# Kernel tuning notes

Measured on AMD Instinct MI355X. Metric: run time of the kernel, lower is better.

## Reference

```python
import jax, jax.numpy as jnp
import numpy as np
from functools import partial

B, T, I, H, S = 256, 512, 128, 256, 4  # batch, seq_len, input_size, hidden_size, num_segments


def setup_inputs() -> dict:
    key = jax.random.key(0)
    ks = jax.random.split(key, 6)
    x = jax.random.normal(ks[0], (B, T, I), dtype=jnp.float32)
    # variable-length sequences so segment indexing floor(t*S/len) is exercised
    lengths = jax.random.randint(ks[1], (B,), T // 2, T + 1)
    mask = jnp.arange(T)[None, :] < lengths[:, None]  # [B, T] bool
    s = 1.0 / np.sqrt(H)  # torch LSTMCell init: U(-1/sqrt(H), 1/sqrt(H))
    W_ih = jax.random.uniform(ks[2], (S, 4 * H, I), minval=-s, maxval=s, dtype=jnp.float32)
    W_hh = jax.random.uniform(ks[3], (S, 4 * H, H), minval=-s, maxval=s, dtype=jnp.float32)
    b_ih = jax.random.uniform(ks[4], (S, 4 * H), minval=-s, maxval=s, dtype=jnp.float32)
    b_hh = jax.random.uniform(ks[5], (S, 4 * H), minval=-s, maxval=s, dtype=jnp.float32)
    return {"x": x, "mask": mask, "W_ih": W_ih, "W_hh": W_hh, "b_ih": b_ih, "b_hh": b_hh}


def _shift_lstm(x, mask, W_ih, W_hh, b_ih, b_hh):
    # dropout is identity in eval mode
    Bb, Tt, _ = x.shape
    lengths = jnp.maximum(mask.astype(jnp.int32).sum(-1), 1)  # clamp_min(1)
    t = jnp.arange(Tt)
    seg = jnp.minimum((t[None, :] * S) // lengths[:, None], S - 1)  # [B, T]
    bias = (b_ih + b_hh)[None]  # [1, S, 4H]

    def step(carry, inputs):
        h, c = carry
        x_t, seg_t, valid = inputs  # [B,I], [B], [B]
        # gates for every segment cell, then pick each sample's segment
        gates = (jnp.einsum('bi,soi->bso', x_t, W_ih)
                 + jnp.einsum('bh,soh->bso', h, W_hh) + bias)  # [B, S, 4H]
        g = jnp.take_along_axis(gates, seg_t[:, None, None], axis=1)[:, 0, :]  # [B, 4H]
        i_g, f_g, g_g, o_g = jnp.split(g, 4, axis=-1)  # torch LSTMCell gate order i,f,g,o
        c_new = jax.nn.sigmoid(f_g) * c + jax.nn.sigmoid(i_g) * jnp.tanh(g_g)
        h_new = jax.nn.sigmoid(o_g) * jnp.tanh(c_new)
        v = valid[:, None]
        h = jnp.where(v, h_new, h)
        c = jnp.where(v, c_new, c)
        out = jnp.where(v, h, jnp.zeros_like(h))  # padded steps stay zero
        return (h, c), out

    h0 = jnp.zeros((Bb, H), dtype=x.dtype)
    c0 = jnp.zeros((Bb, H), dtype=x.dtype)
    xs = (x.transpose(1, 0, 2), seg.T, mask.T)
    _, outs = jax.lax.scan(step, (h0, c0), xs)
    outputs = outs.transpose(1, 0, 2)  # [B, T, H]
    last_idx = (lengths - 1)[:, None, None]
    last_outputs = jnp.take_along_axis(outputs, last_idx, axis=1)[:, 0, :]  # [B, H]
    return outputs, last_outputs


def reference(x, mask, W_ih, W_hh, b_ih, b_hh):
    return _shift_lstm(x, mask, W_ih, W_hh, b_ih, b_hh)
```

## Files before the change

kernel.cpp:

```cpp
#include <hip/hip_runtime.h>
#include <math.h>

#define Bb 256
#define Tt 512
#define Ii 128
#define Hh 256
#define Ss 4
#define G4 1024

#define TILE 8

typedef _Float16 half2t __attribute__((ext_vector_type(2)));
union W16 { uint4 u; half2t h[4]; };
union CV8 { _Float16 h[4]; uint2 u; };

__device__ __forceinline__ float dot8(uint4 w, uint4 hv, float acc) {
  W16 a; a.u = w; W16 b; b.u = hv;
#if __has_builtin(__builtin_amdgcn_fdot2)
  acc = __builtin_amdgcn_fdot2(a.h[0], b.h[0], acc, false);
  acc = __builtin_amdgcn_fdot2(a.h[1], b.h[1], acc, false);
  acc = __builtin_amdgcn_fdot2(a.h[2], b.h[2], acc, false);
  acc = __builtin_amdgcn_fdot2(a.h[3], b.h[3], acc, false);
#else
#pragma unroll
  for (int k = 0; k < 4; k++)
    acc += (float)a.h[k].x * (float)b.h[k].x + (float)a.h[k].y * (float)b.h[k].y;
#endif
  return acc;
}

__global__ void k_len(const int* __restrict__ mask, int* __restrict__ len) {
  int b = blockIdx.x, tid = threadIdx.x;
  int c = (mask[b * Tt + tid] != 0) + (mask[b * Tt + 256 + tid] != 0);
#pragma unroll
  for (int off = 32; off > 0; off >>= 1) c += __shfl_down(c, off, 64);
  __shared__ int red[4];
  if ((tid & 63) == 0) red[tid >> 6] = c;
  __syncthreads();
  if (tid == 0) {
    int t = red[0] + red[1] + red[2] + red[3];
    len[b] = t < 1 ? 1 : t;
  }
}

__global__ void k_tr(const float* __restrict__ W_ih, const float* __restrict__ W_hh,
                     uint4* __restrict__ wt_hh16, uint4* __restrict__ wt_ih16) {
  int id = blockIdx.x * blockDim.x + threadIdx.x;
  const int NH16 = Ss * 32 * G4;
  const int NI16 = Ss * 16 * G4;
  if (id < NH16) {
    int o = id % G4, i8 = (id / G4) % 32, s = id / (G4 * 32);
    const float* src = W_hh + ((size_t)(s * G4 + o)) * Hh + 8 * i8;
    W16 w;
#pragma unroll
    for (int k = 0; k < 4; k++) {
      w.h[k].x = (_Float16)src[2 * k];
      w.h[k].y = (_Float16)src[2 * k + 1];
    }
    wt_hh16[id] = w.u;
  } else if (id < NH16 + NI16) {
    int id3 = id - NH16;
    int o = id3 % G4, i8 = (id3 / G4) % 16, s = id3 / (G4 * 16);
    const float* src = W_ih + ((size_t)(s * G4 + o)) * Ii + 8 * i8;
    W16 w;
#pragma unroll
    for (int k = 0; k < 4; k++) {
      w.h[k].x = (_Float16)src[2 * k];
      w.h[k].y = (_Float16)src[2 * k + 1];
    }
    wt_ih16[id3] = w.u;
  }
}

__global__ __launch_bounds__(512) void k_fused(
    const float* __restrict__ x, const uint4* __restrict__ wt_hh16,
    const uint4* __restrict__ wt_ih16, const float* __restrict__ b_ih,
    const float* __restrict__ b_hh, const int* __restrict__ len,
    float* __restrict__ out) {
  __shared__ __align__(16) uint4 lds_w[19 * 512];
  __shared__ __align__(16) _Float16 xs[TILE * Ii];
  __shared__ __align__(16) _Float16 h_h[Hh];
  __shared__ float f_sh[Hh];
  __shared__ float o_sh[Hh];
  const int b = blockIdx.x;
  const int tid = threadIdx.x;
  const int u = tid & 255;
  const int pr = tid >> 8;
  const int r0 = u + pr * 256;
  const int r1 = r0 + 512;
  const int L = len[b];
  const int tb1 = (L + 3) >> 2;
  const int tb2 = (2 * L + 3) >> 2;
  const int tb3 = (3 * L + 3) >> 2;
  if (pr == 0) h_h[u] = (_Float16)0.f;
  float c = 0.f;
  float* outb = out + (size_t)b * Tt * Hh;
  float* lastb = out + (size_t)Bb * Tt * Hh + (size_t)b * Hh;
  const uint4* h4 = (const uint4*)h_h;
  const uint4* xs4 = (const uint4*)xs;
  uint4 w0v[6];
  uint4 w1v[4];
  int s_cur = -1;
  float xg0[TILE], xg1[TILE];

  for (int t0 = 0; t0 < L; t0 += TILE) {
    if (tid < TILE * Ii / 4) {
      float4 xf = ((const float4*)(x + ((size_t)b * Tt + t0) * Ii))[tid];
      CV8 cv;
      cv.h[0] = (_Float16)xf.x;
      cv.h[1] = (_Float16)xf.y;
      cv.h[2] = (_Float16)xf.z;
      cv.h[3] = (_Float16)xf.w;
      ((uint2*)xs)[tid] = cv.u;
    }
    __syncthreads();

    int segv[TILE];
#pragma unroll
    for (int tt = 0; tt < TILE; tt++) {
      int t = t0 + tt;
      segv[tt] = (t >= tb1) + (t >= tb2) + (t >= tb3);
    }
    const int s_lo = segv[0];
    const int tlast = (t0 + TILE - 1 < L) ? (t0 + TILE - 1) : (L - 1);
    const int s_hi = (tlast >= tb1) + (tlast >= tb2) + (tlast >= tb3);

    for (int s = s_lo; s <= s_hi; s++) {
      float acc0[TILE], acc1[TILE];
#pragma unroll
      for (int tt = 0; tt < TILE; tt++) { acc0[tt] = 0.f; acc1[tt] = 0.f; }
      const uint4* wbi = wt_ih16 + ((size_t)s * 16) * G4;
#pragma unroll 2
      for (int i8 = 0; i8 < 16; i8++) {
        uint4 w0 = wbi[(size_t)i8 * G4 + r0];
        uint4 w1 = wbi[(size_t)i8 * G4 + r1];
#pragma unroll
        for (int tt = 0; tt < TILE; tt++) {
          uint4 hv = xs4[tt * 16 + i8];
          acc0[tt] = dot8(w0, hv, acc0[tt]);
          acc1[tt] = dot8(w1, hv, acc1[tt]);
        }
      }
      float bias0 = b_ih[s * G4 + r0] + b_hh[s * G4 + r0];
      float bias1 = b_ih[s * G4 + r1] + b_hh[s * G4 + r1];
#pragma unroll
      for (int tt = 0; tt < TILE; tt++) {
        if (segv[tt] == s) {
          xg0[tt] = acc0[tt] + bias0;
          xg1[tt] = acc1[tt] + bias1;
        }
      }
    }

#pragma unroll
    for (int tt = 0; tt < TILE; tt++) {
      const int t = t0 + tt;
      if (t < L) {
        const int s = segv[tt];
        if (s != s_cur) {
          s_cur = s;
          const uint4* wb0 = wt_hh16 + (size_t)s * 32 * G4 + r0;
          const uint4* wb1 = wt_hh16 + (size_t)s * 32 * G4 + r1;
#pragma unroll
          for (int j = 0; j < 10; j++) lds_w[j * 512 + tid] = wb0[(size_t)j * G4];
#pragma unroll
          for (int j = 0; j < 9; j++)
            lds_w[(10 + j) * 512 + tid] = wb1[(size_t)j * G4];
#pragma unroll
          for (int k = 0; k < 6; k++) w0v[k] = wb0[(size_t)(10 + k) * G4];
#pragma unroll
          for (int k = 0; k < 4; k++) w1v[k] = wb1[(size_t)(9 + k) * G4];
        }
        const uint4* wbs0 = wt_hh16 + (size_t)s_cur * 32 * G4 + r0;
        const uint4* wbs1 = wt_hh16 + (size_t)s_cur * 32 * G4 + r1;
        uint4 sA[16], sB[19];
        sB[0] = wbs1[(size_t)13 * G4];
        sB[1] = wbs1[(size_t)14 * G4];
        sB[2] = wbs1[(size_t)15 * G4];
        sB[3] = wbs1[(size_t)16 * G4];
        sA[0] = wbs0[(size_t)16 * G4];
        sA[1] = wbs0[(size_t)17 * G4];
        float a0 = xg0[tt], a1 = xg1[tt];
        float a0b = 0.f, a1b = 0.f;
        __syncthreads();
#pragma unroll
        for (int i8 = 0; i8 < 32; i8++) {
          if (i8 == 2) sB[4] = wbs1[(size_t)17 * G4];
          if (i8 == 5) sB[5] = wbs1[(size_t)18 * G4];
          if (i8 == 8) sB[6] = wbs1[(size_t)19 * G4];
          if (i8 == 11) sB[7] = wbs1[(size_t)20 * G4];
          if (i8 >= 13 && i8 <= 23) {
            sB[i8 - 5] = wbs1[(size_t)(i8 + 8) * G4];
            if (i8 >= 14) sA[i8 - 12] = wbs0[(size_t)(i8 + 4) * G4];
          }
          if (i8 == 24) sA[12] = wbs0[(size_t)28 * G4];
          if (i8 == 25) sA[13] = wbs0[(size_t)29 * G4];
          if (i8 == 26) sA[14] = wbs0[(size_t)30 * G4];
          if (i8 == 27) sA[15] = wbs0[(size_t)31 * G4];
          uint4 hv = h4[i8];
          uint4 wA = (i8 < 10) ? lds_w[i8 * 512 + tid]
                   : (i8 < 16) ? w0v[i8 - 10] : sA[i8 - 16];
          uint4 wB = (i8 < 9) ? lds_w[(10 + i8) * 512 + tid]
                   : (i8 < 13) ? w1v[i8 - 9] : sB[i8 - 13];
          if (i8 & 1) { a0b = dot8(wA, hv, a0b); a1b = dot8(wB, hv, a1b); }
          else        { a0  = dot8(wA, hv, a0 ); a1  = dot8(wB, hv, a1 ); }
        }
        a0 += a0b;
        a1 += a1b;
        if (pr == 1) {
          f_sh[u] = 1.f / (1.f + expf(-a0));
          o_sh[u] = 1.f / (1.f + expf(-a1));
        }
        __syncthreads();
        if (pr == 0) {
          float ig = 1.f / (1.f + expf(-a0));
          float gg = tanhf(a1);
          c = f_sh[u] * c + ig * gg;
          float h = o_sh[u] * tanhf(c);
          h_h[u] = (_Float16)h;
          outb[(size_t)t * Hh + u] = h;
          if (t == L - 1) lastb[u] = h;
        }
      }
    }
  }
  {
    const int ztotal = (Tt - L) * (Hh / 4);
    float4* zb = (float4*)(outb + (size_t)L * Hh);
    float4 z; z.x = z.y = z.z = z.w = 0.f;
    for (int i = tid; i < ztotal; i += 512) zb[i] = z;
  }
}

extern "C" void kernel_launch(void* const* d_in, const int* in_sizes, int n_in,
                              void* d_out, int out_size, void* d_ws, size_t ws_size,
                              hipStream_t stream) {
  const float* x = (const float*)d_in[0];
  const int* mask = (const int*)d_in[1];
  const float* W_ih = (const float*)d_in[2];
  const float* W_hh = (const float*)d_in[3];
  const float* b_ih = (const float*)d_in[4];
  const float* b_hh = (const float*)d_in[5];
  float* out = (float*)d_out;
  char* ws = (char*)d_ws;

  const size_t HH16_OFF = 0;
  const size_t HH16_BYTES = (size_t)Ss * 32 * G4 * 16;
  const size_t IH16_OFF = HH16_OFF + HH16_BYTES;
  const size_t IH16_BYTES = (size_t)Ss * 16 * G4 * 16;
  const size_t LEN_OFF = IH16_OFF + IH16_BYTES;

  uint4* wt_hh16 = (uint4*)(ws + HH16_OFF);
  uint4* wt_ih16 = (uint4*)(ws + IH16_OFF);
  int* len = (int*)(ws + LEN_OFF);

  k_len<<<Bb, 256, 0, stream>>>(mask, len);
  k_tr<<<768, 256, 0, stream>>>(W_ih, W_hh, wt_hh16, wt_ih16);
  k_fused<<<Bb, 512, 0, stream>>>(x, wt_hh16, wt_ih16, b_ih, b_hh, len, out);
}
```

Measured before the change: 2.143 ms.

## Pair length-sorted sequences per block to share recurrent weight loads

Adds a rank-sort kernel that orders batch items by length, then has each block process two adjacent-length sequences at once. When both sequences are in the same segment, each W_hh weight fetch feeds two dot products, which halves weight traffic per step and halves the grid to 128 blocks. When the segments differ, a slow path reads both segment weight sets straight from global memory. Risks include longer per-step latency, lower occupancy from the smaller grid, and extra register pressure.

```diff
diff --git a/kernel.cpp b/kernel.cpp
--- a/kernel.cpp
+++ b/kernel.cpp
@@ -7,8 +7,8 @@
 #define Hh 256
 #define Ss 4
 #define G4 1024
-
 #define TILE 8
+
 
 typedef _Float16 half2t __attribute__((ext_vector_type(2)));
 union W16 { uint4 u; half2t h[4]; };
@@ -29,6 +29,8 @@
   return acc;
 }
 
+__device__ __forceinline__ float sigf(float x) { return 1.f / (1.f + expf(-x)); }
+
 __global__ void k_len(const int* __restrict__ mask, int* __restrict__ len) {
   int b = blockIdx.x, tid = threadIdx.x;
   int c = (mask[b * Tt + tid] != 0) + (mask[b * Tt + 256 + tid] != 0);
@@ -41,6 +43,19 @@
     int t = red[0] + red[1] + red[2] + red[3];
     len[b] = t < 1 ? 1 : t;
   }
+}
+
+__global__ void k_sort(const int* __restrict__ len, int* __restrict__ perm) {
+  __shared__ int l[Bb];
+  int tid = threadIdx.x;
+  l[tid] = len[tid];
+  __syncthreads();
+  int me = l[tid], r = 0;
+  for (int j = 0; j < Bb; j++) {
+    int lj = l[j];
+    r += (lj < me) || (lj == me && j < tid);
+  }
+  perm[r] = tid;
 }
 
 __global__ void k_tr(const float* __restrict__ W_ih, const float* __restrict__ W_hh,
@@ -76,78 +91,106 @@
     const float* __restrict__ x, const uint4* __restrict__ wt_hh16,
     const uint4* __restrict__ wt_ih16, const float* __restrict__ b_ih,
     const float* __restrict__ b_hh, const int* __restrict__ len,
-    float* __restrict__ out) {
-  __shared__ __align__(16) uint4 lds_w[19 * 512];
-  __shared__ __align__(16) _Float16 xs[TILE * Ii];
-  __shared__ __align__(16) _Float16 h_h[Hh];
-  __shared__ float f_sh[Hh];
-  __shared__ float o_sh[Hh];
-  const int b = blockIdx.x;
+    const int* __restrict__ perm, float* __restrict__ out) {
+  __shared__ __align__(16) uint4 lds_w[18 * 512];
+  __shared__ __align__(16) _Float16 xs[2][TILE * Ii];
+  __shared__ __align__(16) _Float16 h1_h[Hh], h2_h[Hh];
+  __shared__ float fo_sh[2][2][Hh];
+  const int g = blockIdx.x;
   const int tid = threadIdx.x;
   const int u = tid & 255;
   const int pr = tid >> 8;
   const int r0 = u + pr * 256;
   const int r1 = r0 + 512;
-  const int L = len[b];
-  const int tb1 = (L + 3) >> 2;
-  const int tb2 = (2 * L + 3) >> 2;
-  const int tb3 = (3 * L + 3) >> 2;
-  if (pr == 0) h_h[u] = (_Float16)0.f;
-  float c = 0.f;
-  float* outb = out + (size_t)b * Tt * Hh;
-  float* lastb = out + (size_t)Bb * Tt * Hh + (size_t)b * Hh;
-  const uint4* h4 = (const uint4*)h_h;
-  const uint4* xs4 = (const uint4*)xs;
-  uint4 w0v[6];
-  uint4 w1v[4];
+  const int b1 = perm[2 * g], b2 = perm[2 * g + 1];
+  const int L1 = len[b1], L2v = len[b2];
+  const int A1 = (L1 + 3) >> 2, A2 = (2 * L1 + 3) >> 2, A3 = (3 * L1 + 3) >> 2;
+  const int C1 = (L2v + 3) >> 2, C2 = (2 * L2v + 3) >> 2, C3 = (3 * L2v + 3) >> 2;
+  if (tid < 256) { h1_h[tid] = (_Float16)0.f; }
+  else { h2_h[tid - 256] = (_Float16)0.f; }
+  float c1 = 0.f, c2 = 0.f;
+  float* out1 = out + (size_t)b1 * Tt * Hh;
+  float* out2 = out + (size_t)b2 * Tt * Hh;
+  float* last1 = out + (size_t)Bb * Tt * Hh + (size_t)b1 * Hh;
+  float* last2 = out + (size_t)Bb * Tt * Hh + (size_t)b2 * Hh;
+  const uint4* h4a = (const uint4*)h1_h;
+  const uint4* h4b = (const uint4*)h2_h;
+  const uint4* xs4a = (const uint4*)xs[0];
+  const uint4* xs4b = (const uint4*)xs[1];
   int s_cur = -1;
-  float xg0[TILE], xg1[TILE];
-
-  for (int t0 = 0; t0 < L; t0 += TILE) {
-    if (tid < TILE * Ii / 4) {
-      float4 xf = ((const float4*)(x + ((size_t)b * Tt + t0) * Ii))[tid];
+  float xg0_1[TILE], xg1_1[TILE], xg0_2[TILE], xg1_2[TILE];
+
+  for (int t0 = 0; t0 < L2v; t0 += TILE) {
+    {
+      int m = tid >> 8, f = tid & 255;
+      const float* xb = x + ((size_t)(m ? b2 : b1) * Tt + t0) * Ii;
+      float4 xf = ((const float4*)xb)[f];
       CV8 cv;
       cv.h[0] = (_Float16)xf.x;
       cv.h[1] = (_Float16)xf.y;
       cv.h[2] = (_Float16)xf.z;
       cv.h[3] = (_Float16)xf.w;
-      ((uint2*)xs)[tid] = cv.u;
+      ((uint2*)xs[m])[f] = cv.u;
     }
     __syncthreads();
 
-    int segv[TILE];
-#pragma unroll
-    for (int tt = 0; tt < TILE; tt++) {
-      int t = t0 + tt;
-      segv[tt] = (t >= tb1) + (t >= tb2) + (t >= tb3);
-    }
-    const int s_lo = segv[0];
-    const int tlast = (t0 + TILE - 1 < L) ? (t0 + TILE - 1) : (L - 1);
-    const int s_hi = (tlast >= tb1) + (tlast >= tb2) + (tlast >= tb3);
-
-    for (int s = s_lo; s <= s_hi; s++) {
-      float acc0[TILE], acc1[TILE];
-#pragma unroll
-      for (int tt = 0; tt < TILE; tt++) { acc0[tt] = 0.f; acc1[tt] = 0.f; }
-      const uint4* wbi = wt_ih16 + ((size_t)s * 16) * G4;
+    if (t0 < L1) {
+      int s_lo = (t0 >= A1) + (t0 >= A2) + (t0 >= A3);
+      int te = t0 + TILE - 1;
+      int s_hi = (te >= A1) + (te >= A2) + (te >= A3);
+      for (int s = s_lo; s <= s_hi; s++) {
+        float acc0[TILE], acc1[TILE];
+#pragma unroll
+        for (int tt = 0; tt < TILE; tt++) { acc0[tt] = 0.f; acc1[tt] = 0.f; }
+        const uint4* wbi = wt_ih16 + ((size_t)s * 16) * G4;
 #pragma unroll 2
-      for (int i8 = 0; i8 < 16; i8++) {
-        uint4 w0 = wbi[(size_t)i8 * G4 + r0];
-        uint4 w1 = wbi[(size_t)i8 * G4 + r1];
+        for (int i8 = 0; i8 < 16; i8++) {
+          uint4 w0 = wbi[(size_t)i8 * G4 + r0];
+          uint4 w1 = wbi[(size_t)i8 * G4 + r1];
+#pragma unroll
+          for (int tt = 0; tt < TILE; tt++) {
+            uint4 hv = xs4a[tt * 16 + i8];
+            acc0[tt] = dot8(w0, hv, acc0[tt]);
+            acc1[tt] = dot8(w1, hv, acc1[tt]);
+          }
+        }
+        float bias0 = b_ih[s * G4 + r0] + b_hh[s * G4 + r0];
+        float bias1 = b_ih[s * G4 + r1] + b_hh[s * G4 + r1];
 #pragma unroll
         for (int tt = 0; tt < TILE; tt++) {
-          uint4 hv = xs4[tt * 16 + i8];
-          acc0[tt] = dot8(w0, hv, acc0[tt]);
-          acc1[tt] = dot8(w1, hv, acc1[tt]);
+          int t = t0 + tt;
+          int sg = (t >= A1) + (t >= A2) + (t >= A3);
+          if (sg == s) { xg0_1[tt] = acc0[tt] + bias0; xg1_1[tt] = acc1[tt] + bias1; }
         }
       }
-      float bias0 = b_ih[s * G4 + r0] + b_hh[s * G4 + r0];
-      float bias1 = b_ih[s * G4 + r1] + b_hh[s * G4 + r1];
-#pragma unroll
-      for (int tt = 0; tt < TILE; tt++) {
-        if (segv[tt] == s) {
-          xg0[tt] = acc0[tt] + bias0;
-          xg1[tt] = acc1[tt] + bias1;
+    }
+    {
+      int s_lo = (t0 >= C1) + (t0 >= C2) + (t0 >= C3);
+      int te = t0 + TILE - 1;
+      int s_hi = (te >= C1) + (te >= C2) + (te >= C3);
+      for (int s = s_lo; s <= s_hi; s++) {
+        float acc0[TILE], acc1[TILE];
+#pragma unroll
+        for (int tt = 0; tt < TILE; tt++) { acc0[tt] = 0.f; acc1[tt] = 0.f; }
+        const uint4* wbi = wt_ih16 + ((size_t)s * 16) * G4;
+#pragma unroll 2
+        for (int i8 = 0; i8 < 16; i8++) {
+          uint4 w0 = wbi[(size_t)i8 * G4 + r0];
+          uint4 w1 = wbi[(size_t)i8 * G4 + r1];
+#pragma unroll
+          for (int tt = 0; tt < TILE; tt++) {
+            uint4 hv = xs4b[tt * 16 + i8];
+            acc0[tt] = dot8(w0, hv, acc0[tt]);
+            acc1[tt] = dot8(w1, hv, acc1[tt]);
+          }
+        }
+        float bias0 = b_ih[s * G4 + r0] + b_hh[s * G4 + r0];
+        float bias1 = b_ih[s * G4 + r1] + b_hh[s * G4 + r1];
+#pragma unroll
+        for (int tt = 0; tt < TILE; tt++) {
+          int t = t0 + tt;
+          int sg = (t >= C1) + (t >= C2) + (t >= C3);
+          if (sg == s) { xg0_2[tt] = acc0[tt] + bias0; xg1_2[tt] = acc1[tt] + bias1; }
         }
       }
     }
@@ -155,80 +198,108 @@
 #pragma unroll
     for (int tt = 0; tt < TILE; tt++) {
       const int t = t0 + tt;
-      if (t < L) {
-        const int s = segv[tt];
-        if (s != s_cur) {
-          s_cur = s;
-          const uint4* wb0 = wt_hh16 + (size_t)s * 32 * G4 + r0;
-          const uint4* wb1 = wt_hh16 + (size_t)s * 32 * G4 + r1;
-#pragma unroll
-          for (int j = 0; j < 10; j++) lds_w[j * 512 + tid] = wb0[(size_t)j * G4];
-#pragma unroll
-          for (int j = 0; j < 9; j++)
-            lds_w[(10 + j) * 512 + tid] = wb1[(size_t)j * G4];
-#pragma unroll
-          for (int k = 0; k < 6; k++) w0v[k] = wb0[(size_t)(10 + k) * G4];
-#pragma unroll
-          for (int k = 0; k < 4; k++) w1v[k] = wb1[(size_t)(9 + k) * G4];
-        }
-        const uint4* wbs0 = wt_hh16 + (size_t)s_cur * 32 * G4 + r0;
-        const uint4* wbs1 = wt_hh16 + (size_t)s_cur * 32 * G4 + r1;
-        uint4 sA[16], sB[19];
-        sB[0] = wbs1[(size_t)13 * G4];
-        sB[1] = wbs1[(size_t)14 * G4];
-        sB[2] = wbs1[(size_t)15 * G4];
-        sB[3] = wbs1[(size_t)16 * G4];
-        sA[0] = wbs0[(size_t)16 * G4];
-        sA[1] = wbs0[(size_t)17 * G4];
-        float a0 = xg0[tt], a1 = xg1[tt];
-        float a0b = 0.f, a1b = 0.f;
+      if (t < L2v) {
+        int s2 = (t >= C1) + (t >= C2) + (t >= C3);
+        int s1 = (t >= L1) ? s2 : (t >= A1) + (t >= A2) + (t >= A3);
+        float a0_1 = xg0_1[tt], a1_1 = xg1_1[tt];
+        float a0_2 = xg0_2[tt], a1_2 = xg1_2[tt];
+        uint4 sA[22], sB[24];
+        const uint4* wbs0;
+        const uint4* wbs1;
+        const bool fast = (s1 == s2);
+        if (fast) {
+          if (s2 != s_cur) {
+            s_cur = s2;
+            const uint4* wb0 = wt_hh16 + (size_t)s2 * 32 * G4 + r0;
+            const uint4* wb1 = wt_hh16 + (size_t)s2 * 32 * G4 + r1;
+#pragma unroll
+            for (int j = 0; j < 10; j++) lds_w[j * 512 + tid] = wb0[(size_t)j * G4];
+#pragma unroll
+            for (int j = 0; j < 8; j++)
+              lds_w[(10 + j) * 512 + tid] = wb1[(size_t)j * G4];
+          }
+          wbs0 = wt_hh16 + (size_t)s_cur * 32 * G4 + r0;
+          wbs1 = wt_hh16 + (size_t)s_cur * 32 * G4 + r1;
+          sB[0] = wbs1[(size_t)8 * G4];
+          sB[1] = wbs1[(size_t)9 * G4];
+          sA[0] = wbs0[(size_t)10 * G4];
+          sA[1] = wbs0[(size_t)11 * G4];
+        }
         __syncthreads();
-#pragma unroll
-        for (int i8 = 0; i8 < 32; i8++) {
-          if (i8 == 2) sB[4] = wbs1[(size_t)17 * G4];
-          if (i8 == 5) sB[5] = wbs1[(size_t)18 * G4];
-          if (i8 == 8) sB[6] = wbs1[(size_t)19 * G4];
-          if (i8 == 11) sB[7] = wbs1[(size_t)20 * G4];
-          if (i8 >= 13 && i8 <= 23) {
-            sB[i8 - 5] = wbs1[(size_t)(i8 + 8) * G4];
-            if (i8 >= 14) sA[i8 - 12] = wbs0[(size_t)(i8 + 4) * G4];
-          }
-          if (i8 == 24) sA[12] = wbs0[(size_t)28 * G4];
-          if (i8 == 25) sA[13] = wbs0[(size_t)29 * G4];
-          if (i8 == 26) sA[14] = wbs0[(size_t)30 * G4];
-          if (i8 == 27) sA[15] = wbs0[(size_t)31 * G4];
-          uint4 hv = h4[i8];
-          uint4 wA = (i8 < 10) ? lds_w[i8 * 512 + tid]
-                   : (i8 < 16) ? w0v[i8 - 10] : sA[i8 - 16];
-          uint4 wB = (i8 < 9) ? lds_w[(10 + i8) * 512 + tid]
-                   : (i8 < 13) ? w1v[i8 - 9] : sB[i8 - 13];
-          if (i8 & 1) { a0b = dot8(wA, hv, a0b); a1b = dot8(wB, hv, a1b); }
-          else        { a0  = dot8(wA, hv, a0 ); a1  = dot8(wB, hv, a1 ); }
-        }
-        a0 += a0b;
-        a1 += a1b;
+        if (fast) {
+#pragma unroll
+          for (int i8 = 0; i8 < 32; i8++) {
+            if (i8 == 0) { sB[2] = wbs1[(size_t)10 * G4]; sA[2] = wbs0[(size_t)12 * G4]; }
+            if (i8 == 1) { sB[3] = wbs1[(size_t)11 * G4]; sA[3] = wbs0[(size_t)13 * G4]; }
+            if (i8 == 2) { sB[4] = wbs1[(size_t)12 * G4]; sA[4] = wbs0[(size_t)14 * G4]; }
+            if (i8 == 3) { sB[5] = wbs1[(size_t)13 * G4]; sA[5] = wbs0[(size_t)15 * G4]; }
+            if (i8 == 4) { sB[6] = wbs1[(size_t)14 * G4]; }
+            if (i8 == 8) { sA[6] = wbs0[(size_t)16 * G4]; }
+            if (i8 == 9) { sB[7] = wbs1[(size_t)15 * G4]; }
+            if (i8 >= 10 && i8 <= 24) {
+              sA[i8 - 3] = wbs0[(size_t)(i8 + 7) * G4];
+              sB[i8 - 2] = wbs1[(size_t)(i8 + 6) * G4];
+            }
+            if (i8 == 25) { sB[23] = wbs1[(size_t)31 * G4]; }
+            uint4 hv1 = h4a[i8];
+            uint4 hv2 = h4b[i8];
+            uint4 wA = (i8 < 10) ? lds_w[i8 * 512 + tid] : sA[i8 - 10];
+            uint4 wB = (i8 < 8) ? lds_w[(10 + i8) * 512 + tid] : sB[i8 - 8];
+            a0_1 = dot8(wA, hv1, a0_1);
+            a0_2 = dot8(wA, hv2, a0_2);
+            a1_1 = dot8(wB, hv1, a1_1);
+            a1_2 = dot8(wB, hv2, a1_2);
+          }
+        } else {
+          const uint4* p1 = wt_hh16 + (size_t)s1 * 32 * G4;
+          const uint4* p2 = wt_hh16 + (size_t)s2 * 32 * G4;
+#pragma unroll 2
+          for (int i8 = 0; i8 < 32; i8++) {
+            uint4 hv1 = h4a[i8], hv2 = h4b[i8];
+            uint4 wA1 = p1[(size_t)i8 * G4 + r0], wB1 = p1[(size_t)i8 * G4 + r1];
+            uint4 wA2 = p2[(size_t)i8 * G4 + r0], wB2 = p2[(size_t)i8 * G4 + r1];
+            a0_1 = dot8(wA1, hv1, a0_1);
+            a1_1 = dot8(wB1, hv1, a1_1);
+            a0_2 = dot8(wA2, hv2, a0_2);
+            a1_2 = dot8(wB2, hv2, a1_2);
+          }
+        }
         if (pr == 1) {
-          f_sh[u] = 1.f / (1.f + expf(-a0));
-          o_sh[u] = 1.f / (1.f + expf(-a1));
+          fo_sh[0][0][u] = sigf(a0_1);
+          fo_sh[0][1][u] = sigf(a1_1);
+          fo_sh[1][0][u] = sigf(a0_2);
+          fo_sh[1][1][u] = sigf(a1_2);
         }
         __syncthreads();
         if (pr == 0) {
-          float ig = 1.f / (1.f + expf(-a0));
-          float gg = tanhf(a1);
-          c = f_sh[u] * c + ig * gg;
-          float h = o_sh[u] * tanhf(c);
-          h_h[u] = (_Float16)h;
-          outb[(size_t)t * Hh + u] = h;
-          if (t == L - 1) lastb[u] = h;
+          if (t < L1) {
+            float ig = sigf(a0_1), gg = tanhf(a1_1);
+            c1 = fo_sh[0][0][u] * c1 + ig * gg;
+            float h = fo_sh[0][1][u] * tanhf(c1);
+            h1_h[u] = (_Float16)h;
+            out1[(size_t)t * Hh + u] = h;
+            if (t == L1 - 1) last1[u] = h;
+          }
+          {
+            float ig = sigf(a0_2), gg = tanhf(a1_2);
+            c2 = fo_sh[1][0][u] * c2 + ig * gg;
+            float h = fo_sh[1][1][u] * tanhf(c2);
+            h2_h[u] = (_Float16)h;
+            out2[(size_t)t * Hh + u] = h;
+            if (t == L2v - 1) last2[u] = h;
+          }
         }
       }
     }
   }
   {
-    const int ztotal = (Tt - L) * (Hh / 4);
-    float4* zb = (float4*)(outb + (size_t)L * Hh);
+    int z1 = (Tt - L1) * (Hh / 4);
+    float4* zb = (float4*)(out1 + (size_t)L1 * Hh);
     float4 z; z.x = z.y = z.z = z.w = 0.f;
-    for (int i = tid; i < ztotal; i += 512) zb[i] = z;
+    for (int i = tid; i < z1; i += 512) zb[i] = z;
+    int z2 = (Tt - L2v) * (Hh / 4);
+    float4* zb2 = (float4*)(out2 + (size_t)L2v * Hh);
+    for (int i = tid; i < z2; i += 512) zb2[i] = z;
   }
 }
 
@@ -249,12 +320,16 @@
   const size_t IH16_OFF = HH16_OFF + HH16_BYTES;
   const size_t IH16_BYTES = (size_t)Ss * 16 * G4 * 16;
   const size_t LEN_OFF = IH16_OFF + IH16_BYTES;
+  const size_t PERM_OFF = LEN_OFF + 4096;
 
   uint4* wt_hh16 = (uint4*)(ws + HH16_OFF);
   uint4* wt_ih16 = (uint4*)(ws + IH16_OFF);
   int* len = (int*)(ws + LEN_OFF);
+  int* perm = (int*)(ws + PERM_OFF);
 
   k_len<<<Bb, 256, 0, stream>>>(mask, len);
+  k_sort<<<1, Bb, 0, stream>>>(len, perm);
   k_tr<<<768, 256, 0, stream>>>(W_ih, W_hh, wt_hh16, wt_ih16);
-  k_fused<<<Bb, 512, 0, stream>>>(x, wt_hh16, wt_ih16, b_ih, b_hh, len, out);
-}
+  k_fused<<<Bb / 2, 512, 0, stream>>>(x, wt_hh16, wt_ih16, b_ih, b_hh, len,
+                                      perm, out);
+}
```

Result: slower. 3.293 ms (+53.6%).

## Keep remaining recurrent weights resident in AGPRs instead of reloading each step

Applied to the files above, without the earlier changes.

The W_hh slices that did not fit in LDS or VGPRs were previously re-streamed from global memory on every timestep. They are now loaded once per segment change into accumulation registers (AGPRs) using inline asm, and read back with v_accvgpr_read during the dot-product loop. This removes per-step global/L2 weight traffic from the serial recurrence. The cost is 140 extra AGPRs per thread, which adds register pressure and accvgpr read instructions, and the inline asm may constrain the compiler's scheduling.

```diff
diff --git a/kernel.cpp b/kernel.cpp
--- a/kernel.cpp
+++ b/kernel.cpp
@@ -7,8 +7,8 @@
 #define Hh 256
 #define Ss 4
 #define G4 1024
-
 #define TILE 8
+
 
 typedef _Float16 half2t __attribute__((ext_vector_type(2)));
 union W16 { uint4 u; half2t h[4]; };
@@ -28,6 +28,22 @@
 #endif
   return acc;
 }
+
+#define AGW4(a0_, a1_, a2_, a3_, src)                                        \
+  do {                                                                        \
+    asm volatile("v_accvgpr_write_b32 %0, %1" : "=a"(a0_) : "v"((src).x));   \
+    asm volatile("v_accvgpr_write_b32 %0, %1" : "=a"(a1_) : "v"((src).y));   \
+    asm volatile("v_accvgpr_write_b32 %0, %1" : "=a"(a2_) : "v"((src).z));   \
+    asm volatile("v_accvgpr_write_b32 %0, %1" : "=a"(a3_) : "v"((src).w));   \
+  } while (0)
+
+#define AGR4(dst, a0_, a1_, a2_, a3_)                                        \
+  do {                                                                        \
+    asm volatile("v_accvgpr_read_b32 %0, %1" : "=v"((dst).x) : "a"(a0_));    \
+    asm volatile("v_accvgpr_read_b32 %0, %1" : "=v"((dst).y) : "a"(a1_));    \
+    asm volatile("v_accvgpr_read_b32 %0, %1" : "=v"((dst).z) : "a"(a2_));    \
+    asm volatile("v_accvgpr_read_b32 %0, %1" : "=v"((dst).w) : "a"(a3_));    \
+  } while (0)
 
 __global__ void k_len(const int* __restrict__ mask, int* __restrict__ len) {
   int b = blockIdx.x, tid = threadIdx.x;
@@ -100,6 +116,17 @@
   const uint4* xs4 = (const uint4*)xs;
   uint4 w0v[6];
   uint4 w1v[4];
+  unsigned aA[64];
+  unsigned aB[76];
+  {
+    unsigned z = 0;
+#pragma unroll
+    for (int k = 0; k < 64; k++)
+      asm volatile("v_accvgpr_write_b32 %0, %1" : "=a"(aA[k]) : "v"(z));
+#pragma unroll
+    for (int k = 0; k < 76; k++)
+      asm volatile("v_accvgpr_write_b32 %0, %1" : "=a"(aB[k]) : "v"(z));
+  }
   int s_cur = -1;
   float xg0[TILE], xg1[TILE];
 
@@ -170,38 +197,32 @@
           for (int k = 0; k < 6; k++) w0v[k] = wb0[(size_t)(10 + k) * G4];
 #pragma unroll
           for (int k = 0; k < 4; k++) w1v[k] = wb1[(size_t)(9 + k) * G4];
-        }
-        const uint4* wbs0 = wt_hh16 + (size_t)s_cur * 32 * G4 + r0;
-        const uint4* wbs1 = wt_hh16 + (size_t)s_cur * 32 * G4 + r1;
-        uint4 sA[16], sB[19];
-        sB[0] = wbs1[(size_t)13 * G4];
-        sB[1] = wbs1[(size_t)14 * G4];
-        sB[2] = wbs1[(size_t)15 * G4];
-        sB[3] = wbs1[(size_t)16 * G4];
-        sA[0] = wbs0[(size_t)16 * G4];
-        sA[1] = wbs0[(size_t)17 * G4];
+#pragma unroll
+          for (int k = 0; k < 16; k++) {
+            uint4 w = wb0[(size_t)(16 + k) * G4];
+            AGW4(aA[4 * k + 0], aA[4 * k + 1], aA[4 * k + 2], aA[4 * k + 3], w);
+          }
+#pragma unroll
+          for (int k = 0; k < 19; k++) {
+            uint4 w = wb1[(size_t)(13 + k) * G4];
+            AGW4(aB[4 * k + 0], aB[4 * k + 1], aB[4 * k + 2], aB[4 * k + 3], w);
+          }
+        }
         float a0 = xg0[tt], a1 = xg1[tt];
         float a0b = 0.f, a1b = 0.f;
         __syncthreads();
 #pragma unroll
         for (int i8 = 0; i8 < 32; i8++) {
-          if (i8 == 2) sB[4] = wbs1[(size_t)17 * G4];
-          if (i8 == 5) sB[5] = wbs1[(size_t)18 * G4];
-          if (i8 == 8) sB[6] = wbs1[(size_t)19 * G4];
-          if (i8 == 11) sB[7] = wbs1[(size_t)20 * G4];
-          if (i8 >= 13 && i8 <= 23) {
-            sB[i8 - 5] = wbs1[(size_t)(i8 + 8) * G4];
-            if (i8 >= 14) sA[i8 - 12] = wbs0[(size_t)(i8 + 4) * G4];
-          }
-          if (i8 == 24) sA[12] = wbs0[(size_t)28 * G4];
-          if (i8 == 25) sA[13] = wbs0[(size_t)29 * G4];
-          if (i8 == 26) sA[14] = wbs0[(size_t)30 * G4];
-          if (i8 == 27) sA[15] = wbs0[(size_t)31 * G4];
           uint4 hv = h4[i8];
-          uint4 wA = (i8 < 10) ? lds_w[i8 * 512 + tid]
-                   : (i8 < 16) ? w0v[i8 - 10] : sA[i8 - 16];
-          uint4 wB = (i8 < 9) ? lds_w[(10 + i8) * 512 + tid]
-                   : (i8 < 13) ? w1v[i8 - 9] : sB[i8 - 13];
+          uint4 wA, wB;
+          if (i8 < 10) wA = lds_w[i8 * 512 + tid];
+          else if (i8 < 16) wA = w0v[i8 - 10];
+          else AGR4(wA, aA[4 * (i8 - 16) + 0], aA[4 * (i8 - 16) + 1],
+                    aA[4 * (i8 - 16) + 2], aA[4 * (i8 - 16) + 3]);
+          if (i8 < 9) wB = lds_w[(10 + i8) * 512 + tid];
+          else if (i8 < 13) wB = w1v[i8 - 9];
+          else AGR4(wB, aB[4 * (i8 - 13) + 0], aB[4 * (i8 - 13) + 1],
+                    aB[4 * (i8 - 13) + 2], aB[4 * (i8 - 13) + 3]);
           if (i8 & 1) { a0b = dot8(wA, hv, a0b); a1b = dot8(wB, hv, a1b); }
           else        { a0  = dot8(wA, hv, a0 ); a1  = dot8(wB, hv, a1 ); }
         }
```

Measured after the change: 2.330 ms. 1.09x slower.
